# Kernel optimization log

Measured on AMD Instinct MI355X. Metric: run time of the kernel, lower is better.

Reference implementation:

```python
import jax, jax.numpy as jnp
import numpy as np

NUM_CLASSES = 19
RMI_RADIUS = 3
POOL_SIZE = 3
POOL_STRIDE = 3
IGNORE_INDEX = 255
LOSS_WEIGHT = 1.0


def _avg_pool_nchw(x, k, s):
    # torch F.avg_pool2d with padding=k//2, count_include_pad=True
    p = k // 2
    summed = jax.lax.reduce_window(
        x, 0.0, jax.lax.add,
        window_dimensions=(1, 1, k, k),
        window_strides=(1, 1, s, s),
        padding=[(0, 0), (0, 0), (p, p), (p, p)])
    return summed / float(k * k)


def _map_get_pairs(labels, probs, radius):
    h, w = labels.shape[2], labels.shape[3]
    nh, nw = h - radius + 1, w - radius + 1
    la = jnp.stack([labels[:, :, y:y + nh, x:x + nw]
                    for y in range(radius) for x in range(radius)], axis=2)
    pr = jnp.stack([probs[:, :, y:y + nh, x:x + nw]
                    for y in range(radius) for x in range(radius)], axis=2)
    return la, pr  # (N, C, r*r, nh, nw)


def _log_det_by_cholesky(mat):
    chol = jnp.linalg.cholesky(mat)
    diag = jnp.diagonal(chol, axis1=-2, axis2=-1)
    return 2.0 * jnp.sum(jnp.log(diag + 1e-8), axis=-1)


def _rmi_lower_bound(labels_4d, probs_4d):
    labels_4d = _avg_pool_nchw(labels_4d, POOL_SIZE, POOL_STRIDE)
    probs_4d = _avg_pool_nchw(probs_4d, POOL_SIZE, POOL_STRIDE)
    la, pr = _map_get_pairs(labels_4d, probs_4d, RMI_RADIUS)
    N, C, D = la.shape[:3]
    la = la.reshape(N, C, D, -1)   # (N, C, D, M)
    pr = pr.reshape(N, C, D, -1)
    M = la.shape[-1]
    la = la - la.mean(axis=-1, keepdims=True)
    pr = pr - pr.mean(axis=-1, keepdims=True)
    la_cov = jnp.einsum('ncdm,ncem->ncde', la, la) / M
    pr_cov = jnp.einsum('ncdm,ncem->ncde', pr, pr) / M
    pr_la_cov = jnp.einsum('ncdm,ncem->ncde', pr, la) / M
    eye = jnp.eye(D, dtype=la_cov.dtype)
    la_cov_inv = jnp.linalg.inv(la_cov + eye * 1e-5)
    appro_var = pr_cov - jnp.einsum('ncde,ncef,ncgf->ncdg',
                                    pr_la_cov, la_cov_inv, pr_la_cov)
    appro_var = appro_var + eye * 1e-6
    rmi_per_class = 0.5 * _log_det_by_cholesky(appro_var)  # (N, C)
    rmi_per_class = rmi_per_class.mean(axis=0)             # (C,)
    return jnp.sum(rmi_per_class) / NUM_CLASSES


def setup_inputs() -> dict:
    key = jax.random.key(0)
    k1, k2 = jax.random.split(key)
    cls_score = jax.random.normal(k1, (4, 19, 512, 512), dtype=jnp.float32)
    label = jax.random.randint(k2, (4, 512, 512), 0, NUM_CLASSES, dtype=jnp.int64)
    return {"cls_score": cls_score, "label": label}


def reference(cls_score, label):
    probs = jax.nn.softmax(cls_score.astype(jnp.float32), axis=1)
    valid = (label >= 0) & (label < NUM_CLASSES) & (label != IGNORE_INDEX)
    lbl = jnp.where(valid, label, 0)
    onehot = jax.nn.one_hot(lbl, NUM_CLASSES, dtype=jnp.float32)
    onehot = jnp.transpose(onehot, (0, 3, 1, 2))  # (N, C, H, W)
    vmask = valid[:, None, :, :].astype(jnp.float32)
    onehot = onehot * vmask
    probs = probs * vmask
    loss = _rmi_lower_bound(onehot, probs)
    return LOSS_WEIGHT * loss
```

## Files before the change

kernel.cpp:

```cpp
#include <hip/hip_runtime.h>
#include <math.h>

#define NBATCH 4
#define NCLS   19
#define HWDIM  512
#define HW     (512 * 512)
#define PH     171
#define PHP    176
#define PP2A   (171 * 176)
#define NHW    169
#define MM     (169 * 169)

typedef float f4  __attribute__((ext_vector_type(4)));
typedef float f2v __attribute__((ext_vector_type(2)));

__global__ __launch_bounds__(512) void stage1_pool(
    const float* __restrict__ cls, const int* __restrict__ label,
    float* __restrict__ P, float* __restrict__ L) {
  int n  = blockIdx.x / PH;
  int ph = blockIdx.x - n * PH;
  int col = threadIdx.x;

  float accP[NCLS], accL[NCLS];
#pragma unroll
  for (int c = 0; c < NCLS; ++c) { accP[c] = 0.f; accL[c] = 0.f; }

#pragma unroll
  for (int i = 0; i < 3; ++i) {
    int r = 3 * ph - 1 + i;
    if (r < 0 || r >= HWDIM) continue;
    int lb = label[((size_t)n * HWDIM + r) * HWDIM + col];
    const float* base = cls + (size_t)n * NCLS * HW + (size_t)r * HWDIM + col;
    float v[NCLS];
    float mx = -INFINITY;
#pragma unroll
    for (int c = 0; c < NCLS; ++c) {
      v[c] = base[(size_t)c * HW];
      mx = fmaxf(mx, v[c]);
    }
    float se = 0.f;
#pragma unroll
    for (int c = 0; c < NCLS; ++c) {
      v[c] = expf(v[c] - mx);
      se += v[c];
    }
    if (lb >= 0 && lb < NCLS) {
      float inv = 1.f / se;
#pragma unroll
      for (int c = 0; c < NCLS; ++c) {
        accP[c] += v[c] * inv;
        accL[c] += (lb == c) ? 1.f : 0.f;
      }
    }
  }

  __shared__ float xbP[4][516];
  __shared__ float xbL[4][516];
  const float inv9 = 1.f / 9.f;
#pragma unroll
  for (int c0 = 0; c0 < NCLS; c0 += 4) {
    int nc_round = (NCLS - c0) < 4 ? (NCLS - c0) : 4;
#pragma unroll
    for (int cc = 0; cc < 4; ++cc) {
      if (cc < nc_round) {
        xbP[cc][1 + col] = accP[(c0 + cc) < NCLS ? (c0 + cc) : 0];
        xbL[cc][1 + col] = accL[(c0 + cc) < NCLS ? (c0 + cc) : 0];
        if (col == 0) { xbP[cc][0] = 0.f; xbL[cc][0] = 0.f; }
      }
    }
    __syncthreads();
    if (col < PH) {
      int pw = col;
#pragma unroll
      for (int cc = 0; cc < 4; ++cc) {
        if (cc < nc_round) {
          int c = c0 + cc;
          float sP = xbP[cc][3 * pw] + xbP[cc][3 * pw + 1] + xbP[cc][3 * pw + 2];
          float sL = xbL[cc][3 * pw] + xbL[cc][3 * pw + 1] + xbL[cc][3 * pw + 2];
          size_t o = ((size_t)(n * NCLS + c)) * PP2A + (size_t)ph * PHP + pw;
          P[o] = sP * inv9;
          L[o] = sL * inv9;
        }
      }
    } else if (col < PHP) {
#pragma unroll
      for (int cc = 0; cc < 4; ++cc) {
        if (cc < nc_round) {
          int c = c0 + cc;
          size_t o = ((size_t)(n * NCLS + c)) * PP2A + (size_t)ph * PHP + col;
          P[o] = 0.f;
          L[o] = 0.f;
        }
      }
    }
    __syncthreads();
  }
}

template <int MODE, int NA>
__device__ __forceinline__ void epilogue(const f2v (&acc2)[NA], float* red,
                                         float* __restrict__ covp, int nc) {
  int lane = threadIdx.x & 63;
  int wid  = threadIdx.x >> 6;
#pragma unroll
  for (int k = 0; k < NA; ++k) {
    float v = acc2[k].x + acc2[k].y;
    v += __shfl_down(v, 32, 64);
    v += __shfl_down(v, 16, 64);
    v += __shfl_down(v, 8, 64);
    if (lane < 8) red[(wid * 8 + lane) * 84 + k] = v;
  }
  __syncthreads();
  int tid = threadIdx.x;
  if (tid < NA) {
    float sm = 0.f;
#pragma unroll
    for (int w = 0; w < 64; ++w) sm += red[w * 84 + tid];
    int off;
    if (MODE == 0)      off = (tid < 9) ? tid : 18 + (tid - 9);
    else if (MODE == 1) off = (tid < 9) ? 9 + tid : 63 + (tid - 9);
    else                off = 108 + tid;
    covp[(size_t)nc * 192 + off] = sm;
  }
}

template <int MODE>
__device__ __forceinline__ void mom_self(const float* __restrict__ X,
                                         float* __restrict__ covp, int nc,
                                         float* red) {
  f2v acc2[54];
#pragma unroll
  for (int k = 0; k < 54; ++k) acc2[k] = (f2v){0.f, 0.f};

  int tid = threadIdx.x;
  if (tid < 462) {
    int b = tid / 42, s = tid - b * 42;
    int x0 = 4 * s;
    int y0 = (NHW * b) / 11;
    int y1 = (NHW * (b + 1)) / 11;

    f2v w[3][5];
#pragma unroll
    for (int r = 0; r < 3; ++r) {
      f4  a  = *(const f4*)(X + (y0 + r) * PHP + x0);
      f2v bb = *(const f2v*)(X + (y0 + r) * PHP + x0 + 4);
      w[r][0] = (f2v){a.x, a.y}; w[r][1] = (f2v){a.y, a.z};
      w[r][2] = (f2v){a.z, a.w}; w[r][3] = (f2v){a.w, bb.x};
      w[r][4] = bb;
    }

    for (int y = y0; y < y1; ++y) {
      int yn = (y + 3 <= PH - 1) ? (y + 3) : (PH - 1);
      f4  a  = *(const f4*)(X + yn * PHP + x0);
      f2v bb = *(const f2v*)(X + yn * PHP + x0 + 4);

#pragma unroll
      for (int d = 0; d < 9; ++d) {
        acc2[d] += w[d / 3][d % 3];
        acc2[d] += w[d / 3][(d % 3) + 2];
      }
      {
        int k = 9;
#pragma unroll
        for (int d = 0; d < 9; ++d)
#pragma unroll
          for (int e = d; e < 9; ++e) {
            acc2[k] += w[d / 3][d % 3] * w[e / 3][e % 3];
            acc2[k] += w[d / 3][(d % 3) + 2] * w[e / 3][(e % 3) + 2];
            ++k;
          }
      }
#pragma unroll
      for (int j = 0; j < 5; ++j) { w[0][j] = w[1][j]; w[1][j] = w[2][j]; }
      w[2][0] = (f2v){a.x, a.y}; w[2][1] = (f2v){a.y, a.z};
      w[2][2] = (f2v){a.z, a.w}; w[2][3] = (f2v){a.w, bb.x};
      w[2][4] = bb;
    }
  } else if (tid < 473) {
    int b  = tid - 462;
    int y0 = (NHW * b) / 11;
    int y1 = (NHW * (b + 1)) / 11;
    float t[3][3];
#pragma unroll
    for (int r = 0; r < 3; ++r)
#pragma unroll
      for (int c = 0; c < 3; ++c) t[r][c] = X[(y0 + r) * PHP + 168 + c];
    for (int y = y0; y < y1; ++y) {
      int yn = (y + 3 <= PH - 1) ? (y + 3) : (PH - 1);
      float n0 = X[yn * PHP + 168], n1 = X[yn * PHP + 169],
            n2 = X[yn * PHP + 170];
#pragma unroll
      for (int d = 0; d < 9; ++d) acc2[d].x += t[d / 3][d % 3];
      {
        int k = 9;
#pragma unroll
        for (int d = 0; d < 9; ++d)
#pragma unroll
          for (int e = d; e < 9; ++e) {
            acc2[k].x += t[d / 3][d % 3] * t[e / 3][e % 3];
            ++k;
          }
      }
#pragma unroll
      for (int c = 0; c < 3; ++c) { t[0][c] = t[1][c]; t[1][c] = t[2][c]; }
      t[2][0] = n0; t[2][1] = n1; t[2][2] = n2;
    }
  }
  epilogue<MODE, 54>(acc2, red, covp, nc);
}

__device__ __forceinline__ void mom_cross(const float* __restrict__ Pp,
                                          const float* __restrict__ Lp,
                                          float* __restrict__ covp, int nc,
                                          float* red) {
  f2v acc2[81];
#pragma unroll
  for (int k = 0; k < 81; ++k) acc2[k] = (f2v){0.f, 0.f};

  int tid = threadIdx.x;
  if (tid < 504) {
    int b = tid / 84, s = tid - b * 84;
    int x0 = 2 * s;
    int y0 = (NHW * b) / 6;
    int y1 = (NHW * (b + 1)) / 6;

    f2v wp[3][3], wl[3][3];
#pragma unroll
    for (int r = 0; r < 3; ++r) {
      f2v p01 = *(const f2v*)(Pp + (y0 + r) * PHP + x0);
      f2v p23 = *(const f2v*)(Pp + (y0 + r) * PHP + x0 + 2);
      wp[r][0] = p01; wp[r][1] = (f2v){p01.y, p23.x}; wp[r][2] = p23;
      f2v l01 = *(const f2v*)(Lp + (y0 + r) * PHP + x0);
      f2v l23 = *(const f2v*)(Lp + (y0 + r) * PHP + x0 + 2);
      wl[r][0] = l01; wl[r][1] = (f2v){l01.y, l23.x}; wl[r][2] = l23;
    }

    for (int y = y0; y < y1; ++y) {
      int yn = (y + 3 <= PH - 1) ? (y + 3) : (PH - 1);
      f2v p01 = *(const f2v*)(Pp + yn * PHP + x0);
      f2v p23 = *(const f2v*)(Pp + yn * PHP + x0 + 2);
      f2v l01 = *(const f2v*)(Lp + yn * PHP + x0);
      f2v l23 = *(const f2v*)(Lp + yn * PHP + x0 + 2);

#pragma unroll
      for (int d = 0; d < 9; ++d)
#pragma unroll
        for (int e = 0; e < 9; ++e)
          acc2[d * 9 + e] += wp[d / 3][d % 3] * wl[e / 3][e % 3];

#pragma unroll
      for (int j = 0; j < 3; ++j) {
        wp[0][j] = wp[1][j]; wp[1][j] = wp[2][j];
        wl[0][j] = wl[1][j]; wl[1][j] = wl[2][j];
      }
      wp[2][0] = p01; wp[2][1] = (f2v){p01.y, p23.x}; wp[2][2] = p23;
      wl[2][0] = l01; wl[2][1] = (f2v){l01.y, l23.x}; wl[2][2] = l23;
    }
  } else if (tid < 510) {
    int b  = tid - 504;
    int y0 = (NHW * b) / 6;
    int y1 = (NHW * (b + 1)) / 6;
    float tp[3][3], tl[3][3];
#pragma unroll
    for (int r = 0; r < 3; ++r)
#pragma unroll
      for (int c = 0; c < 3; ++c) {
        tp[r][c] = Pp[(y0 + r) * PHP + 168 + c];
        tl[r][c] = Lp[(y0 + r) * PHP + 168 + c];
      }
    for (int y = y0; y < y1; ++y) {
      int yn = (y + 3 <= PH - 1) ? (y + 3) : (PH - 1);
      float np0 = Pp[yn * PHP + 168], np1 = Pp[yn * PHP + 169],
            np2 = Pp[yn * PHP + 170];
      float nl0 = Lp[yn * PHP + 168], nl1 = Lp[yn * PHP + 169],
            nl2 = Lp[yn * PHP + 170];
#pragma unroll
      for (int d = 0; d < 9; ++d)
#pragma unroll
        for (int e = 0; e < 9; ++e)
          acc2[d * 9 + e].x += tp[d / 3][d % 3] * tl[e / 3][e % 3];
#pragma unroll
      for (int c = 0; c < 3; ++c) {
        tp[0][c] = tp[1][c]; tp[1][c] = tp[2][c];
        tl[0][c] = tl[1][c]; tl[1][c] = tl[2][c];
      }
      tp[2][0] = np0; tp[2][1] = np1; tp[2][2] = np2;
      tl[2][0] = nl0; tl[2][1] = nl1; tl[2][2] = nl2;
    }
  }
  epilogue<2, 81>(acc2, red, covp, nc);
}

__global__ __launch_bounds__(512) void stage2_mom(
    const float* __restrict__ P, const float* __restrict__ L,
    float* __restrict__ covp) {
  __shared__ float red[64 * 84];
  int nc = blockIdx.x;
  const float* Pp = P + (size_t)nc * PP2A;
  const float* Lp = L + (size_t)nc * PP2A;
  if (blockIdx.y == 0)      mom_self<0>(Lp, covp, nc, red);
  else if (blockIdx.y == 1) mom_self<1>(Pp, covp, nc, red);
  else                      mom_cross(Pp, Lp, covp, nc, red);
}

__global__ __launch_bounds__(64) void stage3_rmi(float* __restrict__ covp) {
  int nc  = blockIdx.x;
  int tid = threadIdx.x;
  const float* s = covp + (size_t)nc * 192;
  __shared__ double lc[81], pc[81], plc[81], mla[9], mpr[9];
  const double Minv = 1.0 / (double)MM;

  if (tid < 9)       mla[tid]     = (double)s[tid] * Minv;
  else if (tid < 18) mpr[tid - 9] = (double)s[tid] * Minv;
  __syncthreads();

  for (int e = tid; e < 81; e += 64) {
    int r = e / 9, c = e - 9 * (e / 9);
    int lo = r < c ? r : c, hi = r < c ? c : r;
    int k = lo * 9 - lo * (lo - 1) / 2 + (hi - lo);
    double a = (double)s[18 + k] * Minv - mla[r] * mla[c];
    if (r == c) a += 1e-5;
    lc[e] = a;
    pc[e] = (double)s[63 + k] * Minv - mpr[r] * mpr[c];
    plc[e] = (double)s[108 + e] * Minv - mpr[r] * mla[c];
  }
  __syncthreads();

  for (int j = 0; j < 9; ++j) {
    if (tid == 0) lc[j * 9 + j] = sqrt(lc[j * 9 + j]);
    __syncthreads();
    if (tid > j && tid < 9) lc[tid * 9 + j] /= lc[j * 9 + j];
    __syncthreads();
    if (tid > j && tid < 9) {
      double lij = lc[tid * 9 + j];
      for (int k = j + 1; k <= tid; ++k) lc[tid * 9 + k] -= lij * lc[k * 9 + j];
    }
    __syncthreads();
  }

  if (tid < 9) {
    int d = tid;
    for (int j = 0; j < 9; ++j) {
      double t = plc[d * 9 + j];
      for (int k = 0; k < j; ++k) t -= plc[d * 9 + k] * lc[j * 9 + k];
      plc[d * 9 + j] = t / lc[j * 9 + j];
    }
  }
  __syncthreads();

  for (int e = tid; e < 81; e += 64) {
    int r = e / 9, c = e - 9 * (e / 9);
    double a = pc[e];
    for (int f = 0; f < 9; ++f) a -= plc[r * 9 + f] * plc[c * 9 + f];
    if (r == c) a += 1e-6;
    pc[e] = a;
  }
  __syncthreads();

  for (int j = 0; j < 9; ++j) {
    if (tid == 0) pc[j * 9 + j] = sqrt(pc[j * 9 + j]);
    __syncthreads();
    if (tid > j && tid < 9) pc[tid * 9 + j] /= pc[j * 9 + j];
    __syncthreads();
    if (tid > j && tid < 9) {
      double lij = pc[tid * 9 + j];
      for (int k = j + 1; k <= tid; ++k) pc[tid * 9 + k] -= lij * pc[k * 9 + j];
    }
    __syncthreads();
  }

  if (tid == 0) {
    double sl = 0.0;
    for (int j = 0; j < 9; ++j) sl += log(pc[j * 9 + j] + 1e-8);
    *(double*)(covp + (size_t)nc * 192 + 190) = sl;
  }
}

__global__ __launch_bounds__(64) void stage4_reduce(
    const float* __restrict__ covp, float* __restrict__ out) {
  int tid = threadIdx.x;
  double v = 0.0;
  if (tid < NBATCH * NCLS)
    v = *(const double*)(covp + (size_t)tid * 192 + 190);
  if (tid + 64 < NBATCH * NCLS)
    v += *(const double*)(covp + (size_t)(tid + 64) * 192 + 190);
#pragma unroll
  for (int o = 32; o > 0; o >>= 1) v += __shfl_down(v, o, 64);
  if (tid == 0) out[0] = (float)(v / (double)(NBATCH * NCLS));
}

extern "C" void kernel_launch(void* const* d_in, const int* in_sizes, int n_in,
                              void* d_out, int out_size, void* d_ws, size_t ws_size,
                              hipStream_t stream) {
  const float* cls  = (const float*)d_in[0];
  const int* label  = (const int*)d_in[1];
  float* out = (float*)d_out;

  float* P    = (float*)d_ws;
  float* L    = P + (size_t)NBATCH * NCLS * PP2A;
  float* covp = L + (size_t)NBATCH * NCLS * PP2A;

  stage1_pool<<<NBATCH * PH, 512, 0, stream>>>(cls, label, P, L);
  dim3 g2(NBATCH * NCLS, 3, 1);
  stage2_mom<<<g2, 512, 0, stream>>>(P, L, covp);
  stage3_rmi<<<NBATCH * NCLS, 64, 0, stream>>>(covp);
  stage4_reduce<<<1, 64, 0, stream>>>(covp, out);
}
```

Baseline: 76.29 us.

## Batch pooling loads, use fast exp, and rotate row buffers in moment loops

Stage 1 now loads all three input rows of logits and labels before doing any softmax work. It uses __expf and a mask multiply instead of a branch, and processes 10 classes per shared-memory round instead of 4, which cuts the number of barriers. The self and cross moment loops replace the per-row shift of the sliding window with a four-buffer rotating scheme unrolled by four, so the next row's load is issued before the FMAs on the current rows. This aims to hide memory latency and remove register moves, at the cost of more register pressure and a little lower exp precision.

Result: faster. 72.49 us (-5.0%).

```diff
diff --git a/kernel.cpp b/kernel.cpp
--- a/kernel.cpp
+++ b/kernel.cpp
@@ -21,48 +21,57 @@
   int ph = blockIdx.x - n * PH;
   int col = threadIdx.x;
 
-  float accP[NCLS], accL[NCLS];
-#pragma unroll
-  for (int c = 0; c < NCLS; ++c) { accP[c] = 0.f; accL[c] = 0.f; }
-
+  float vv[3][NCLS];
+  int lbs[3];
 #pragma unroll
   for (int i = 0; i < 3; ++i) {
     int r = 3 * ph - 1 + i;
-    if (r < 0 || r >= HWDIM) continue;
-    int lb = label[((size_t)n * HWDIM + r) * HWDIM + col];
-    const float* base = cls + (size_t)n * NCLS * HW + (size_t)r * HWDIM + col;
-    float v[NCLS];
-    float mx = -INFINITY;
+    bool ok = (r >= 0) && (r < HWDIM);
+    if (ok) {
+      lbs[i] = label[((size_t)n * HWDIM + r) * HWDIM + col];
+      const float* base = cls + (size_t)n * NCLS * HW + (size_t)r * HWDIM + col;
+#pragma unroll
+      for (int c = 0; c < NCLS; ++c) vv[i][c] = base[(size_t)c * HW];
+    } else {
+      lbs[i] = -1;
+#pragma unroll
+      for (int c = 0; c < NCLS; ++c) vv[i][c] = 0.f;
+    }
+  }
+
+  float accP[NCLS], accL[NCLS];
+#pragma unroll
+  for (int c = 0; c < NCLS; ++c) { accP[c] = 0.f; accL[c] = 0.f; }
+#pragma unroll
+  for (int i = 0; i < 3; ++i) {
+    int lb = lbs[i];
+    float mx = vv[i][0];
+#pragma unroll
+    for (int c = 1; c < NCLS; ++c) mx = fmaxf(mx, vv[i][c]);
+    float se = 0.f;
+    float ex[NCLS];
 #pragma unroll
     for (int c = 0; c < NCLS; ++c) {
-      v[c] = base[(size_t)c * HW];
-      mx = fmaxf(mx, v[c]);
-    }
-    float se = 0.f;
+      ex[c] = __expf(vv[i][c] - mx);
+      se += ex[c];
+    }
+    float m = (lb >= 0 && lb < NCLS) ? 1.f : 0.f;
+    float inv = m / se;
 #pragma unroll
     for (int c = 0; c < NCLS; ++c) {
-      v[c] = expf(v[c] - mx);
-      se += v[c];
-    }
-    if (lb >= 0 && lb < NCLS) {
-      float inv = 1.f / se;
-#pragma unroll
-      for (int c = 0; c < NCLS; ++c) {
-        accP[c] += v[c] * inv;
-        accL[c] += (lb == c) ? 1.f : 0.f;
-      }
-    }
-  }
-
-  __shared__ float xbP[4][516];
-  __shared__ float xbL[4][516];
+      accP[c] += ex[c] * inv;
+      accL[c] += (lb == c) ? 1.f : 0.f;
+    }
+  }
+
+  __shared__ float xbP[10][516];
+  __shared__ float xbL[10][516];
   const float inv9 = 1.f / 9.f;
 #pragma unroll
-  for (int c0 = 0; c0 < NCLS; c0 += 4) {
-    int nc_round = (NCLS - c0) < 4 ? (NCLS - c0) : 4;
-#pragma unroll
-    for (int cc = 0; cc < 4; ++cc) {
-      if (cc < nc_round) {
+  for (int c0 = 0; c0 < NCLS; c0 += 10) {
+#pragma unroll
+    for (int cc = 0; cc < 10; ++cc) {
+      if (c0 + cc < NCLS) {
         xbP[cc][1 + col] = accP[(c0 + cc) < NCLS ? (c0 + cc) : 0];
         xbL[cc][1 + col] = accL[(c0 + cc) < NCLS ? (c0 + cc) : 0];
         if (col == 0) { xbP[cc][0] = 0.f; xbL[cc][0] = 0.f; }
@@ -72,8 +81,8 @@
     if (col < PH) {
       int pw = col;
 #pragma unroll
-      for (int cc = 0; cc < 4; ++cc) {
-        if (cc < nc_round) {
+      for (int cc = 0; cc < 10; ++cc) {
+        if (c0 + cc < NCLS) {
           int c = c0 + cc;
           float sP = xbP[cc][3 * pw] + xbP[cc][3 * pw + 1] + xbP[cc][3 * pw + 2];
           float sL = xbL[cc][3 * pw] + xbL[cc][3 * pw + 1] + xbL[cc][3 * pw + 2];
@@ -84,8 +93,8 @@
       }
     } else if (col < PHP) {
 #pragma unroll
-      for (int cc = 0; cc < 4; ++cc) {
-        if (cc < nc_round) {
+      for (int cc = 0; cc < 10; ++cc) {
+        if (c0 + cc < NCLS) {
           int c = c0 + cc;
           size_t o = ((size_t)(n * NCLS + c)) * PP2A + (size_t)ph * PHP + col;
           P[o] = 0.f;
@@ -124,6 +133,43 @@
   }
 }
 
+__device__ __forceinline__ void fma_self_triple(f2v (&acc2)[54],
+    const f2v (&r0)[5], const f2v (&r1)[5], const f2v (&r2)[5]) {
+#define RP(d, off) ((d) < 3 ? r0[(d) % 3 + (off)] \
+                 : (d) < 6 ? r1[(d) % 3 + (off)] : r2[(d) % 3 + (off)])
+#pragma unroll
+  for (int d = 0; d < 9; ++d) {
+    acc2[d] += RP(d, 0);
+    acc2[d] += RP(d, 2);
+  }
+  {
+    int k = 9;
+#pragma unroll
+    for (int d = 0; d < 9; ++d)
+#pragma unroll
+      for (int e = d; e < 9; ++e) {
+        acc2[k] += RP(d, 0) * RP(e, 0);
+        acc2[k] += RP(d, 2) * RP(e, 2);
+        ++k;
+      }
+  }
+#undef RP
+}
+
+__device__ __forceinline__ void fma_cross_triple(f2v (&acc2)[81],
+    const f2v (&p0)[3], const f2v (&p1)[3], const f2v (&p2)[3],
+    const f2v (&l0)[3], const f2v (&l1)[3], const f2v (&l2)[3]) {
+#define QP(d) ((d) < 3 ? p0[(d) % 3] : (d) < 6 ? p1[(d) % 3] : p2[(d) % 3])
+#define QL(e) ((e) < 3 ? l0[(e) % 3] : (e) < 6 ? l1[(e) % 3] : l2[(e) % 3])
+#pragma unroll
+  for (int d = 0; d < 9; ++d)
+#pragma unroll
+    for (int e = 0; e < 9; ++e)
+      acc2[d * 9 + e] += QP(d) * QL(e);
+#undef QP
+#undef QL
+}
+
 template <int MODE>
 __device__ __forceinline__ void mom_self(const float* __restrict__ X,
                                          float* __restrict__ covp, int nc,
@@ -139,43 +185,30 @@
     int y0 = (NHW * b) / 11;
     int y1 = (NHW * (b + 1)) / 11;
 
-    f2v w[3][5];
-#pragma unroll
-    for (int r = 0; r < 3; ++r) {
-      f4  a  = *(const f4*)(X + (y0 + r) * PHP + x0);
-      f2v bb = *(const f2v*)(X + (y0 + r) * PHP + x0 + 4);
-      w[r][0] = (f2v){a.x, a.y}; w[r][1] = (f2v){a.y, a.z};
-      w[r][2] = (f2v){a.z, a.w}; w[r][3] = (f2v){a.w, bb.x};
-      w[r][4] = bb;
-    }
-
-    for (int y = y0; y < y1; ++y) {
-      int yn = (y + 3 <= PH - 1) ? (y + 3) : (PH - 1);
-      f4  a  = *(const f4*)(X + yn * PHP + x0);
-      f2v bb = *(const f2v*)(X + yn * PHP + x0 + 4);
-
-#pragma unroll
-      for (int d = 0; d < 9; ++d) {
-        acc2[d] += w[d / 3][d % 3];
-        acc2[d] += w[d / 3][(d % 3) + 2];
-      }
-      {
-        int k = 9;
-#pragma unroll
-        for (int d = 0; d < 9; ++d)
-#pragma unroll
-          for (int e = d; e < 9; ++e) {
-            acc2[k] += w[d / 3][d % 3] * w[e / 3][e % 3];
-            acc2[k] += w[d / 3][(d % 3) + 2] * w[e / 3][(e % 3) + 2];
-            ++k;
-          }
-      }
-#pragma unroll
-      for (int j = 0; j < 5; ++j) { w[0][j] = w[1][j]; w[1][j] = w[2][j]; }
-      w[2][0] = (f2v){a.x, a.y}; w[2][1] = (f2v){a.y, a.z};
-      w[2][2] = (f2v){a.z, a.w}; w[2][3] = (f2v){a.w, bb.x};
-      w[2][4] = bb;
-    }
+    f2v s0[5], s1[5], s2[5], s3[5];
+    auto ldr = [&](f2v (&dst)[5], int row) {
+      if (row > PH - 1) row = PH - 1;
+      f4  a  = *(const f4*)(X + row * PHP + x0);
+      f2v bb = *(const f2v*)(X + row * PHP + x0 + 4);
+      dst[0] = (f2v){a.x, a.y}; dst[1] = (f2v){a.y, a.z};
+      dst[2] = (f2v){a.z, a.w}; dst[3] = (f2v){a.w, bb.x};
+      dst[4] = bb;
+    };
+    ldr(s0, y0); ldr(s1, y0 + 1); ldr(s2, y0 + 2);
+
+    int y = y0;
+    int span = y1 - y0;
+    int nf = span & ~3;
+    for (int i = 0; i < nf; i += 4, y += 4) {
+      ldr(s3, y + 3); fma_self_triple(acc2, s0, s1, s2);
+      ldr(s0, y + 4); fma_self_triple(acc2, s1, s2, s3);
+      ldr(s1, y + 5); fma_self_triple(acc2, s2, s3, s0);
+      ldr(s2, y + 6); fma_self_triple(acc2, s3, s0, s1);
+    }
+    int r = span & 3;
+    if (r > 0) { ldr(s3, y + 3); fma_self_triple(acc2, s0, s1, s2); ++y; }
+    if (r > 1) { ldr(s0, y + 3); fma_self_triple(acc2, s1, s2, s3); ++y; }
+    if (r > 2) { ldr(s1, y + 3); fma_self_triple(acc2, s2, s3, s0); ++y; }
   } else if (tid < 473) {
     int b  = tid - 462;
     int y0 = (NHW * b) / 11;
@@ -224,38 +257,32 @@
     int y0 = (NHW * b) / 6;
     int y1 = (NHW * (b + 1)) / 6;
 
-    f2v wp[3][3], wl[3][3];
-#pragma unroll
-    for (int r = 0; r < 3; ++r) {
-      f2v p01 = *(const f2v*)(Pp + (y0 + r) * PHP + x0);
-      f2v p23 = *(const f2v*)(Pp + (y0 + r) * PHP + x0 + 2);
-      wp[r][0] = p01; wp[r][1] = (f2v){p01.y, p23.x}; wp[r][2] = p23;
-      f2v l01 = *(const f2v*)(Lp + (y0 + r) * PHP + x0);
-      f2v l23 = *(const f2v*)(Lp + (y0 + r) * PHP + x0 + 2);
-      wl[r][0] = l01; wl[r][1] = (f2v){l01.y, l23.x}; wl[r][2] = l23;
-    }
-
-    for (int y = y0; y < y1; ++y) {
-      int yn = (y + 3 <= PH - 1) ? (y + 3) : (PH - 1);
-      f2v p01 = *(const f2v*)(Pp + yn * PHP + x0);
-      f2v p23 = *(const f2v*)(Pp + yn * PHP + x0 + 2);
-      f2v l01 = *(const f2v*)(Lp + yn * PHP + x0);
-      f2v l23 = *(const f2v*)(Lp + yn * PHP + x0 + 2);
-
-#pragma unroll
-      for (int d = 0; d < 9; ++d)
-#pragma unroll
-        for (int e = 0; e < 9; ++e)
-          acc2[d * 9 + e] += wp[d / 3][d % 3] * wl[e / 3][e % 3];
-
-#pragma unroll
-      for (int j = 0; j < 3; ++j) {
-        wp[0][j] = wp[1][j]; wp[1][j] = wp[2][j];
-        wl[0][j] = wl[1][j]; wl[1][j] = wl[2][j];
-      }
-      wp[2][0] = p01; wp[2][1] = (f2v){p01.y, p23.x}; wp[2][2] = p23;
-      wl[2][0] = l01; wl[2][1] = (f2v){l01.y, l23.x}; wl[2][2] = l23;
-    }
+    f2v p0[3], p1[3], p2[3], p3[3];
+    f2v l0[3], l1[3], l2[3], l3[3];
+    auto ldc = [&](f2v (&dp)[3], f2v (&dl)[3], int row) {
+      if (row > PH - 1) row = PH - 1;
+      f2v a = *(const f2v*)(Pp + row * PHP + x0);
+      f2v bb = *(const f2v*)(Pp + row * PHP + x0 + 2);
+      dp[0] = a; dp[1] = (f2v){a.y, bb.x}; dp[2] = bb;
+      f2v c = *(const f2v*)(Lp + row * PHP + x0);
+      f2v d = *(const f2v*)(Lp + row * PHP + x0 + 2);
+      dl[0] = c; dl[1] = (f2v){c.y, d.x}; dl[2] = d;
+    };
+    ldc(p0, l0, y0); ldc(p1, l1, y0 + 1); ldc(p2, l2, y0 + 2);
+
+    int y = y0;
+    int span = y1 - y0;
+    int nf = span & ~3;
+    for (int i = 0; i < nf; i += 4, y += 4) {
+      ldc(p3, l3, y + 3); fma_cross_triple(acc2, p0, p1, p2, l0, l1, l2);
+      ldc(p0, l0, y + 4); fma_cross_triple(acc2, p1, p2, p3, l1, l2, l3);
+      ldc(p1, l1, y + 5); fma_cross_triple(acc2, p2, p3, p0, l2, l3, l0);
+      ldc(p2, l2, y + 6); fma_cross_triple(acc2, p3, p0, p1, l3, l0, l1);
+    }
+    int r = span & 3;
+    if (r > 0) { ldc(p3, l3, y + 3); fma_cross_triple(acc2, p0, p1, p2, l0, l1, l2); ++y; }
+    if (r > 1) { ldc(p0, l0, y + 3); fma_cross_triple(acc2, p1, p2, p3, l1, l2, l3); ++y; }
+    if (r > 2) { ldc(p1, l1, y + 3); fma_cross_triple(acc2, p2, p3, p0, l2, l3, l0); ++y; }
   } else if (tid < 510) {
     int b  = tid - 504;
     int y0 = (NHW * b) / 6;
```
